# Kernel optimization log

Hardware: AMD Instinct MI355X
Metric: run time of the kernel (lower is better)

## Reference

```python
import jax, jax.numpy as jnp
import numpy as np

DIM = 1024
NUM_HEADS = 16
HEAD_DIM = DIM // NUM_HEADS
SCALE = 1.0 / np.sqrt(HEAD_DIM)
B, S = 2, 2048


def setup_inputs() -> dict:
    key = jax.random.key(0)
    ks = jax.random.split(key, 10)
    std = 1.0 / np.sqrt(DIM)
    return {
        "x": jax.random.normal(ks[0], (B, S, DIM), dtype=jnp.float32),
        "Wq": jax.random.normal(ks[1], (DIM, DIM), dtype=jnp.float32) * std,
        "bq": jnp.zeros((DIM,), dtype=jnp.float32),
        "Wk": jax.random.normal(ks[2], (DIM, DIM), dtype=jnp.float32) * std,
        "bk": jnp.zeros((DIM,), dtype=jnp.float32),
        "Wv": jax.random.normal(ks[3], (DIM, DIM), dtype=jnp.float32) * std,
        "bv": jnp.zeros((DIM,), dtype=jnp.float32),
        "Wo": jax.random.normal(ks[4], (DIM, DIM), dtype=jnp.float32) * std,
        "bo": jnp.zeros((DIM,), dtype=jnp.float32),
        "mobius_weight": jax.random.normal(ks[5], (1,), dtype=jnp.float32) * 0.01,
    }


def _split_heads(t):
    b, s, _ = t.shape
    return t.reshape(b, s, NUM_HEADS, HEAD_DIM).transpose(0, 2, 1, 3)  # bhsd


def reference(x, Wq, bq, Wk, bk, Wv, bv, Wo, bo, mobius_weight):
    q = _split_heads(x @ Wq.T + bq)
    k = _split_heads(x @ Wk.T + bk)
    v = _split_heads(x @ Wv.T + bv)

    # similarity: plain QK^T
    similarity = jnp.einsum('bhqd,bhkd->bhqk', q, k)
    # mobius cross-term: q_omega . k_pi + q_pi . k_omega
    h = HEAD_DIM // 2
    q_om, q_pi = q[..., :h], q[..., h:]
    k_om, k_pi = k[..., :h], k[..., h:]
    mobius = jnp.einsum('bhqd,bhkd->bhqk', q_om, k_pi) + \
             jnp.einsum('bhqd,bhkd->bhqk', q_pi, k_om)

    incidence = (similarity + mobius_weight[0] * mobius) * SCALE
    attn = jax.nn.softmax(incidence, axis=-1)
    out = jnp.einsum('bhqk,bhkd->bhqd', attn, v)
    out = out.transpose(0, 2, 1, 3).reshape(x.shape[0], x.shape[1], DIM)
    return out @ Wo.T + bo
```

## Files before the change

### kernel.cpp

```cpp
#include <hip/hip_runtime.h>


typedef __attribute__((ext_vector_type(8))) short short8;
typedef __attribute__((ext_vector_type(4))) short s16x4;
typedef __attribute__((ext_vector_type(4))) float f32x4;
typedef __attribute__((ext_vector_type(16))) float f32x16;
typedef __attribute__((ext_vector_type(8))) __bf16 bf16x8;
typedef __attribute__((ext_vector_type(4))) unsigned uint4v;

__device__ __forceinline__ float exp2fa(float x) {
  return __builtin_amdgcn_exp2f(x);
}
__device__ __forceinline__ short f2bf(float f) {
  unsigned u = __builtin_bit_cast(unsigned, f);
  u = u + 0x7fffu + ((u >> 16) & 1u);
  return (short)(u >> 16);
}
__device__ __forceinline__ f32x4 mfma16(bf16x8 a, bf16x8 b, f32x4 c) {
  return __builtin_amdgcn_mfma_f32_16x16x32_bf16(a, b, c, 0, 0, 0);
}
__device__ __forceinline__ f32x16 mfma32(bf16x8 a, bf16x8 b, f32x16 c) {
  return __builtin_amdgcn_mfma_f32_32x32x16_bf16(a, b, c, 0, 0, 0);
}
__device__ __forceinline__ void gload_lds16(const void* g, void* l) {
  __builtin_amdgcn_global_load_lds(
      (const __attribute__((address_space(1))) unsigned int*)g,
      (__attribute__((address_space(3))) unsigned int*)l, 16, 0, 0);
}
__device__ __forceinline__ unsigned pkbf(float a, float b) {
  unsigned r;
  asm("v_cvt_pk_bf16_f32 %0, %1, %2" : "=v"(r) : "v"(a), "v"(b));
  return r;
}
__device__ __forceinline__ void plswap(unsigned& a, unsigned& b) {
  asm volatile("v_permlane32_swap_b32 %0, %1" : "+v"(a), "+v"(b));
}
__device__ __forceinline__ bf16x8 pack8(float x0, float x1, float x2, float x3,
                                        float x4, float x5, float x6, float x7) {
  unsigned a0 = pkbf(x0, x1), a1 = pkbf(x2, x3);
  unsigned a2 = pkbf(x4, x5), a3 = pkbf(x6, x7);
  plswap(a0, a2);
  plswap(a1, a3);
  uint4v u = {a0, a1, a2, a3};
  return __builtin_bit_cast(bf16x8, u);
}

__global__ void cast_all_kernel(const float* x, const float* w0, const float* w1,
                                const float* w2, const float* w3, short* xo,
                                short* o0, short* o1, short* o2, short* o3) {
  const float* in; short* out;
  const int r = blockIdx.y;
  size_t off;
  if (r < 4) { in = x; out = xo; off = (size_t)r * 131072; }
  else {
    switch (r) {
      case 4: in = w0; out = o0; break;
      case 5: in = w1; out = o1; break;
      case 6: in = w2; out = o2; break;
      default: in = w3; out = o3; break;
    }
    off = 0;
  }
  const size_t i = off + blockIdx.x * 256 + threadIdx.x;
  const float4* p = (const float4*)in;
  float4 a = p[2 * i], b = p[2 * i + 1];
  short8 o;
  o[0] = f2bf(a.x); o[1] = f2bf(a.y); o[2] = f2bf(a.z); o[3] = f2bf(a.w);
  o[4] = f2bf(b.x); o[5] = f2bf(b.y); o[6] = f2bf(b.z); o[7] = f2bf(b.w);
  ((short8*)out)[i] = o;
}

constexpr int GK = 1024, GN = 1024;
constexpr float QSCALE = 0.125f * 1.44269504088896340736f;

template <int EP>
__device__ __forceinline__ void gemm_body(char* lds, const short* __restrict__ A,
                                          const short* __restrict__ W,
                                          const float* __restrict__ bias,
                                          void* __restrict__ C,
                                          const float* __restrict__ mwp) {
  const int tid = threadIdx.x;
  const int l = tid & 63, w = tid >> 6;
  const int wr = w >> 1, wc = w & 1;
  const int m0 = blockIdx.y * 128, n0 = blockIdx.x * 128;

  f32x4 acc[4][4] = {};

  const int rg = l >> 3, c8 = l & 7;
  for (int kb = 0; kb < GK / 64; ++kb) {
    const int k0 = kb * 64;
#pragma unroll
    for (int i = 0; i < 4; ++i) {
      const int ra = i * 32 + w * 8 + rg;
      gload_lds16(A + (size_t)(m0 + ra) * GK + k0 + ((c8 ^ (ra & 7)) * 8),
                  lds + (i * 32 + w * 8) * 128);
      gload_lds16(W + (size_t)(n0 + ra) * GK + k0 + ((c8 ^ (ra & 7)) * 8),
                  lds + 16384 + (i * 32 + w * 8) * 128);
    }
    __syncthreads();
#pragma unroll
    for (int ks = 0; ks < 2; ++ks) {
      bf16x8 af[4], bfr[4];
      const int chunk = ks * 4 + (l >> 4);
#pragma unroll
      for (int mf = 0; mf < 4; ++mf) {
        const int mt = wr * 64 + mf * 16 + (l & 15);
        af[mf] = *(const bf16x8*)(lds + mt * 128 + ((chunk ^ (mt & 7)) * 16));
      }
#pragma unroll
      for (int nf = 0; nf < 4; ++nf) {
        const int nt = wc * 64 + nf * 16 + (l & 15);
        bfr[nf] = *(const bf16x8*)(lds + 16384 + nt * 128 + ((chunk ^ (nt & 7)) * 16));
      }
#pragma unroll
      for (int mf = 0; mf < 4; ++mf)
#pragma unroll
        for (int nf = 0; nf < 4; ++nf)
          acc[mf][nf] = mfma16(af[mf], bfr[nf], acc[mf][nf]);
    }
    __syncthreads();
  }

  const float mwv = (EP == 1) ? mwp[0] : 0.f;
#pragma unroll
  for (int mf = 0; mf < 4; ++mf)
#pragma unroll
    for (int nf = 0; nf < 4; ++nf) {
      const int n = n0 + wc * 64 + nf * 16 + (l & 15);
      const int mb = m0 + wr * 64 + mf * 16 + (l >> 4) * 4;
      if (EP == 1) {
        const float bv = bias[n], bv2 = bias[n ^ 32];
        const int h = n >> 6, c = (n >> 3) & 7, j = n & 7;
#pragma unroll
        for (int r = 0; r < 4; ++r) {
          const int m = mb + r;
          const int b = m >> 11, s = m & 2047;
          const float v =
              acc[mf][nf][r] + bv + mwv * (acc[mf][nf ^ 2][r] + bv2);
          ((short*)C)[(size_t)(b * 16 + h) * 131072 + (s >> 5) * 2048 + c * 256 +
                      (s & 31) * 8 + j] = f2bf(v);
        }
      } else if (EP == 2) {
        const int h = n >> 6, w2 = (n >> 5) & 1, dlo = n & 31;
        s16x4 v;
#pragma unroll
        for (int r = 0; r < 4; ++r) v[r] = f2bf(acc[mf][nf][r] + bias[n]);
        const int b = mb >> 11, s = mb & 2047;
        *(s16x4*)((short*)C + (size_t)(b * 16 + h) * 131072 + (s >> 6) * 4096 +
                  w2 * 2048 + ((s >> 3) & 7) * 256 + dlo * 8 + (s & 7)) = v;
      } else {
        const float bv = bias[n];
#pragma unroll
        for (int r = 0; r < 4; ++r) {
          const int m = mb + r;
          float v = acc[mf][nf][r] + bv;
          if (EP == 0) v *= QSCALE;
          if (EP == 3)
            ((float*)C)[(size_t)m * GN + n] = v;
          else
            ((short*)C)[(size_t)m * GN + n] = f2bf(v);
        }
      }
    }
}

__global__ __launch_bounds__(256) void gemm_qkv_kernel(
    const short* __restrict__ A, const short* Wq, const short* Wk, const short* Wv,
    const float* bq, const float* bk, const float* bv, short* q, short* kf,
    short* vf, const float* mw) {
  __shared__ __align__(16) char lds[32768];
  if (blockIdx.z == 0) gemm_body<0>(lds, A, Wq, bq, q, nullptr);
  else if (blockIdx.z == 1) gemm_body<1>(lds, A, Wk, bk, kf, mw);
  else gemm_body<2>(lds, A, Wv, bv, vf, nullptr);
}

__global__ __launch_bounds__(256) void gemm_out_kernel(const short* __restrict__ A,
                                                       const short* __restrict__ W,
                                                       const float* __restrict__ bias,
                                                       float* __restrict__ C) {
  __shared__ __align__(16) char lds[32768];
  gemm_body<3>(lds, A, W, bias, C, nullptr);
}

__global__ __launch_bounds__(256, 3) void attn_kernel(const short* __restrict__ Q,
                                                      const short* __restrict__ Kf,
                                                      const short* __restrict__ Vf,
                                                      short* __restrict__ O) {
  constexpr int S = 2048;
  __shared__ float mbuf[2][32][64];
  __shared__ float lbuf[64];
  const int tid = threadIdx.x;
  const int l = tid & 63, w = tid >> 6;
  const int lo = l & 31, hi = l >> 5;
  const int wq = w & 1, par = w >> 1;
  const int bid = blockIdx.x;
  const int sub = bid >> 3;
  const int x = sub & 31;
  const int y = (bid & 7) * 4 + (sub >> 5);
  const int b = y >> 4, h = y & 15;
  const int q0 = x * 64 + wq * 32;
  const size_t base = (size_t)b * S * 1024 + h * 64;
  const size_t fbase = (size_t)y * 131072;

  bf16x8 qf[4];
  {
    const short* qp = Q + base + (size_t)(q0 + lo) * 1024 + hi * 8;
#pragma unroll
    for (int ds = 0; ds < 4; ++ds) qf[ds] = *(const bf16x8*)(qp + ds * 16);
  }

  const int voff = hi * 256 + lo * 8;
  const short* kp = Kf + fbase + par * 4096 + voff;
  const short* vp = Vf + fbase + par * 4096 + voff;

  bf16x8 kf[8], vf[8];
#pragma unroll
  for (int ds = 0; ds < 4; ++ds) {
    kf[ds]     = *(const bf16x8*)(kp + ds * 512);
    kf[4 + ds] = *(const bf16x8*)(kp + 2048 + ds * 512);
    vf[ds]     = *(const bf16x8*)(vp + ds * 512);
    vf[4 + ds] = *(const bf16x8*)(vp + 2048 + ds * 512);
  }

  f32x16 o0 = {}, o1 = {};
  float lrow = 0.f;

  for (int i = 0; i < S / 128; ++i) {
    f32x16 st0 = {}, st1 = {};
    __builtin_amdgcn_s_setprio(1);
#pragma unroll
    for (int ds = 0; ds < 4; ++ds) {
      st0 = mfma32(kf[ds], qf[ds], st0);
      st1 = mfma32(kf[4 + ds], qf[ds], st1);
    }
    __builtin_amdgcn_s_setprio(0);
    if (i + 1 < S / 128) {
      kp += 8192;
#pragma unroll
      for (int ds = 0; ds < 4; ++ds) {
        kf[ds]     = *(const bf16x8*)(kp + ds * 512);
        kf[4 + ds] = *(const bf16x8*)(kp + 2048 + ds * 512);
      }
    }

#pragma unroll
    for (int r = 0; r < 16; ++r) st0[r] = exp2fa(st0[r]);
#pragma unroll
    for (int r = 0; r < 16; ++r) st1[r] = exp2fa(st1[r]);
    float ts[8];
#pragma unroll
    for (int r = 0; r < 8; ++r)
      ts[r] = (st0[r] + st0[r + 8]) + (st1[r] + st1[r + 8]);
#pragma unroll
    for (int d = 4; d >= 1; d >>= 1)
#pragma unroll
      for (int r = 0; r < 4; ++r)
        if (r < d) ts[r] += ts[r + d];
    lrow += ts[0] + __shfl_xor(ts[0], 32);

    bf16x8 pf[4];
    pf[0] = pack8(st0[0], st0[1], st0[2], st0[3], st0[4], st0[5], st0[6], st0[7]);
    pf[1] = pack8(st0[8], st0[9], st0[10], st0[11], st0[12], st0[13], st0[14], st0[15]);
    pf[2] = pack8(st1[0], st1[1], st1[2], st1[3], st1[4], st1[5], st1[6], st1[7]);
    pf[3] = pack8(st1[8], st1[9], st1[10], st1[11], st1[12], st1[13], st1[14], st1[15]);

    __builtin_amdgcn_s_setprio(1);
#pragma unroll
    for (int kv = 0; kv < 4; ++kv) {
      o0 = mfma32(vf[kv], pf[kv], o0);
      o1 = mfma32(vf[4 + kv], pf[kv], o1);
    }
    __builtin_amdgcn_s_setprio(0);
    if (i + 1 < S / 128) {
      vp += 8192;
#pragma unroll
      for (int kv = 0; kv < 4; ++kv) {
        vf[kv]     = *(const bf16x8*)(vp + kv * 512);
        vf[4 + kv] = *(const bf16x8*)(vp + 2048 + kv * 512);
      }
    }
  }

  if (par == 1) {
#pragma unroll
    for (int g = 0; g < 4; ++g) {
      const int c0 = (2 * g + hi) ^ (lo & 15);
      const int c1 = (8 + 2 * g + hi) ^ (lo & 15);
      f32x4 v0, v1;
#pragma unroll
      for (int r = 0; r < 4; ++r) { v0[r] = o0[g * 4 + r]; v1[r] = o1[g * 4 + r]; }
      *(f32x4*)(&mbuf[wq][lo][c0 * 4]) = v0;
      *(f32x4*)(&mbuf[wq][lo][c1 * 4]) = v1;
    }
    if (hi == 0) lbuf[wq * 32 + lo] = lrow;
  }
  __syncthreads();
  if (par == 0) {
#pragma unroll
    for (int g = 0; g < 4; ++g) {
      const int c0 = (2 * g + hi) ^ (lo & 15);
      const int c1 = (8 + 2 * g + hi) ^ (lo & 15);
      f32x4 v0 = *(const f32x4*)(&mbuf[wq][lo][c0 * 4]);
      f32x4 v1 = *(const f32x4*)(&mbuf[wq][lo][c1 * 4]);
#pragma unroll
      for (int r = 0; r < 4; ++r) { o0[g * 4 + r] += v0[r]; o1[g * 4 + r] += v1[r]; }
    }
    const float inv = 1.0f / (lrow + lbuf[wq * 32 + lo]);
    short* Op = O + base + (size_t)(q0 + lo) * 1024;
#pragma unroll
    for (int g = 0; g < 4; ++g) {
      s16x4 v0, v1;
#pragma unroll
      for (int r = 0; r < 4; ++r) {
        v0[r] = f2bf(o0[g * 4 + r] * inv);
        v1[r] = f2bf(o1[g * 4 + r] * inv);
      }
      *(s16x4*)(Op + 8 * g + 4 * hi) = v0;
      *(s16x4*)(Op + 32 + 8 * g + 4 * hi) = v1;
    }
  }
}

extern "C" void kernel_launch(void* const* d_in, const int* in_sizes, int n_in,
                              void* d_out, int out_size, void* d_ws, size_t ws_size,
                              hipStream_t stream) {
  const float* x  = (const float*)d_in[0];
  const float* Wq = (const float*)d_in[1];
  const float* bq = (const float*)d_in[2];
  const float* Wk = (const float*)d_in[3];
  const float* bk = (const float*)d_in[4];
  const float* Wv = (const float*)d_in[5];
  const float* bv = (const float*)d_in[6];
  const float* Wo = (const float*)d_in[7];
  const float* bo = (const float*)d_in[8];
  const float* mw = (const float*)d_in[9];
  float* out = (float*)d_out;
  char* ws = (char*)d_ws;
  const size_t MB = (size_t)1 << 20;

  short* xb  = (short*)(ws + 0 * MB);
  short* wqb = (short*)(ws + 8 * MB);
  short* wkb = (short*)(ws + 10 * MB);
  short* wvb = (short*)(ws + 12 * MB);
  short* wob = (short*)(ws + 14 * MB);
  short* qb  = (short*)(ws + 16 * MB);
  short* kfb = (short*)(ws + 24 * MB);
  short* vfb = (short*)(ws + 32 * MB);
  short* ob  = (short*)(ws + 40 * MB);

  cast_all_kernel<<<dim3(512, 8), 256, 0, stream>>>(x, Wq, Wk, Wv, Wo, xb, wqb,
                                                    wkb, wvb, wob);
  gemm_qkv_kernel<<<dim3(8, 32, 3), 256, 0, stream>>>(xb, wqb, wkb, wvb, bq, bk, bv,
                                                      qb, kfb, vfb, mw);
  attn_kernel<<<1024, 256, 0, stream>>>(qb, kfb, vfb, ob);
  gemm_out_kernel<<<dim3(8, 32), 256, 0, stream>>>(ob, wob, bo, out);
}
```

Baseline: 126.0 us.

## Software-pipeline attention loop so next QK^T MFMAs overlap softmax and PV

Restructures the attention main loop with a prologue and epilogue so that the QK^T MFMAs for tile i+1 are issued in the same priority block as the PV MFMAs for tile i. K and V loads for the next tile are batched together. The per-iteration cross-lane shuffle for the row sum is deferred to a single shuffle after the loop. This aims to hide exp and packing latency behind matrix work, at the cost of higher register pressure from live st and pf values together with prefetched K and V.

```diff
diff --git a/kernel.cpp b/kernel.cpp
--- a/kernel.cpp
+++ b/kernel.cpp
@@ -187,6 +187,7 @@
                                                       const short* __restrict__ Vf,
                                                       short* __restrict__ O) {
   constexpr int S = 2048;
+  constexpr int NT = S / 128;
   __shared__ float mbuf[2][32][64];
   __shared__ float lbuf[64];
   const int tid = threadIdx.x;
@@ -225,24 +226,22 @@
   f32x16 o0 = {}, o1 = {};
   float lrow = 0.f;
 
-  for (int i = 0; i < S / 128; ++i) {
-    f32x16 st0 = {}, st1 = {};
-    __builtin_amdgcn_s_setprio(1);
-#pragma unroll
-    for (int ds = 0; ds < 4; ++ds) {
-      st0 = mfma32(kf[ds], qf[ds], st0);
-      st1 = mfma32(kf[4 + ds], qf[ds], st1);
-    }
-    __builtin_amdgcn_s_setprio(0);
-    if (i + 1 < S / 128) {
-      kp += 8192;
-#pragma unroll
-      for (int ds = 0; ds < 4; ++ds) {
-        kf[ds]     = *(const bf16x8*)(kp + ds * 512);
-        kf[4 + ds] = *(const bf16x8*)(kp + 2048 + ds * 512);
-      }
-    }
-
+  f32x16 st0 = {}, st1 = {};
+  __builtin_amdgcn_s_setprio(1);
+#pragma unroll
+  for (int ds = 0; ds < 4; ++ds) {
+    st0 = mfma32(kf[ds], qf[ds], st0);
+    st1 = mfma32(kf[4 + ds], qf[ds], st1);
+  }
+  __builtin_amdgcn_s_setprio(0);
+  kp += 8192;
+#pragma unroll
+  for (int ds = 0; ds < 4; ++ds) {
+    kf[ds]     = *(const bf16x8*)(kp + ds * 512);
+    kf[4 + ds] = *(const bf16x8*)(kp + 2048 + ds * 512);
+  }
+
+  for (int i = 0; i < NT - 1; ++i) {
 #pragma unroll
     for (int r = 0; r < 16; ++r) st0[r] = exp2fa(st0[r]);
 #pragma unroll
@@ -256,7 +255,7 @@
 #pragma unroll
       for (int r = 0; r < 4; ++r)
         if (r < d) ts[r] += ts[r + d];
-    lrow += ts[0] + __shfl_xor(ts[0], 32);
+    lrow += ts[0];
 
     bf16x8 pf[4];
     pf[0] = pack8(st0[0], st0[1], st0[2], st0[3], st0[4], st0[5], st0[6], st0[7]);
@@ -266,20 +265,61 @@
 
     __builtin_amdgcn_s_setprio(1);
 #pragma unroll
+    for (int r = 0; r < 16; ++r) { st0[r] = 0.f; st1[r] = 0.f; }
+#pragma unroll
+    for (int ds = 0; ds < 4; ++ds) {
+      st0 = mfma32(kf[ds], qf[ds], st0);
+      st1 = mfma32(kf[4 + ds], qf[ds], st1);
+    }
+#pragma unroll
     for (int kv = 0; kv < 4; ++kv) {
       o0 = mfma32(vf[kv], pf[kv], o0);
       o1 = mfma32(vf[4 + kv], pf[kv], o1);
     }
     __builtin_amdgcn_s_setprio(0);
-    if (i + 1 < S / 128) {
-      vp += 8192;
-#pragma unroll
-      for (int kv = 0; kv < 4; ++kv) {
-        vf[kv]     = *(const bf16x8*)(vp + kv * 512);
-        vf[4 + kv] = *(const bf16x8*)(vp + 2048 + kv * 512);
-      }
-    }
-  }
+
+    kp += 8192;
+    vp += 8192;
+#pragma unroll
+    for (int ds = 0; ds < 4; ++ds) {
+      kf[ds]     = *(const bf16x8*)(kp + ds * 512);
+      kf[4 + ds] = *(const bf16x8*)(kp + 2048 + ds * 512);
+      vf[ds]     = *(const bf16x8*)(vp + ds * 512);
+      vf[4 + ds] = *(const bf16x8*)(vp + 2048 + ds * 512);
+    }
+  }
+
+  {
+#pragma unroll
+    for (int r = 0; r < 16; ++r) st0[r] = exp2fa(st0[r]);
+#pragma unroll
+    for (int r = 0; r < 16; ++r) st1[r] = exp2fa(st1[r]);
+    float ts[8];
+#pragma unroll
+    for (int r = 0; r < 8; ++r)
+      ts[r] = (st0[r] + st0[r + 8]) + (st1[r] + st1[r + 8]);
+#pragma unroll
+    for (int d = 4; d >= 1; d >>= 1)
+#pragma unroll
+      for (int r = 0; r < 4; ++r)
+        if (r < d) ts[r] += ts[r + d];
+    lrow += ts[0];
+
+    bf16x8 pf[4];
+    pf[0] = pack8(st0[0], st0[1], st0[2], st0[3], st0[4], st0[5], st0[6], st0[7]);
+    pf[1] = pack8(st0[8], st0[9], st0[10], st0[11], st0[12], st0[13], st0[14], st0[15]);
+    pf[2] = pack8(st1[0], st1[1], st1[2], st1[3], st1[4], st1[5], st1[6], st1[7]);
+    pf[3] = pack8(st1[8], st1[9], st1[10], st1[11], st1[12], st1[13], st1[14], st1[15]);
+    __builtin_amdgcn_s_setprio(1);
+#pragma unroll
+    for (int kv = 0; kv < 4; ++kv) {
+      o0 = mfma32(vf[kv], pf[kv], o0);
+      o1 = mfma32(vf[4 + kv], pf[kv], o1);
+    }
+    __builtin_amdgcn_s_setprio(0);
+  }
+
+  lrow += __shfl_xor(lrow, 32);
 
   if (par == 1) {
 #pragma unroll
```

New measurement: 126.3 us. Within noise of the previous version (+0.2%).
